# Kernel tuning notes

Measured on AMD Instinct MI355X. Metric: run time of the kernel, lower is better.

## Reference

```python
import jax, jax.numpy as jnp
import numpy as np

NUM_HEADS = 16
EMB = 1024
HEAD = 64
SEQ = 2048
BATCH = 4


def setup_inputs() -> dict:
    key = jax.random.key(0)
    ks = jax.random.split(key, 6)
    s = EMB ** -0.5
    x = jax.random.normal(ks[0], (BATCH, SEQ, EMB), dtype=jnp.float32)
    # per-head projection weights stacked: [H, E, D] (Linear(emb, head, bias=False) per head)
    Wq = jax.random.normal(ks[1], (NUM_HEADS, EMB, HEAD), dtype=jnp.float32) * s
    Wk = jax.random.normal(ks[2], (NUM_HEADS, EMB, HEAD), dtype=jnp.float32) * s
    Wv = jax.random.normal(ks[3], (NUM_HEADS, EMB, HEAD), dtype=jnp.float32) * s
    # output projection Linear(head*num_heads, emb): weight [E, H*D], bias [E]
    Wo = jax.random.normal(ks[4], (EMB, NUM_HEADS * HEAD), dtype=jnp.float32) * ((NUM_HEADS * HEAD) ** -0.5)
    bo = jax.random.normal(ks[5], (EMB,), dtype=jnp.float32) * 0.01
    return {"x": x, "Wq": Wq, "Wk": Wk, "Wv": Wv, "Wo": Wo, "bo": bo}


def reference(x, Wq, Wk, Wv, Wo, bo):
    B, S, E = x.shape
    scale = HEAD ** -0.5
    # batched per-head projections: [B, H, S, D]
    q = jnp.einsum('bse,hed->bhsd', x, Wq)
    k = jnp.einsum('bse,hed->bhsd', x, Wk)
    v = jnp.einsum('bse,hed->bhsd', x, Wv)
    scores = jnp.einsum('bhqd,bhkd->bhqk', q, k) * scale
    causal = jnp.tril(jnp.ones((S, S), dtype=bool))
    scores = jnp.where(causal, scores, jnp.finfo(scores.dtype).min)
    attn = jax.nn.softmax(scores, axis=-1)  # dropout disabled (eval/deterministic)
    ctx = jnp.einsum('bhqk,bhkd->bhqd', attn, v)
    # concat heads along last dim (head-major order, matching torch.cat)
    concat = ctx.transpose(0, 2, 1, 3).reshape(B, S, NUM_HEADS * HEAD)
    out = concat @ Wo.T + bo
    return out
```

## Files before the change

### kernel.cpp

```cpp
#include <hip/hip_runtime.h>

#define NHEADS 16
#define EMB 1024
#define HDIM 64
#define SEQ 2048
#define BATCH 4

typedef unsigned short u16;
typedef __attribute__((ext_vector_type(8))) __bf16 bf16x8;
typedef __attribute__((ext_vector_type(4))) float f32x4;

#if __has_builtin(__builtin_amdgcn_exp2f)
#define EXP2(x) __builtin_amdgcn_exp2f(x)
#else
#define EXP2(x) __expf((x)*0.69314718056f)
#endif
#define CL2E 0.18033688011112042f

__device__ __forceinline__ u16 f2bf(float f) {
  union { float f; unsigned u; } v; v.f = f;
  unsigned r = v.u + 0x7fffu + ((v.u >> 16) & 1u);
  return (u16)(r >> 16);
}
__device__ __forceinline__ unsigned pk2bf(float a, float b) {
  union { __bf16 h[2]; unsigned u; } x;
  x.h[0] = (__bf16)a; x.h[1] = (__bf16)b; return x.u;
}
__device__ __forceinline__ void gl16(const void* g, void* l) {
  __builtin_amdgcn_global_load_lds(
      (const __attribute__((address_space(1))) unsigned*)g,
      (__attribute__((address_space(3))) unsigned*)l, 16, 0, 0);
}

__global__ __launch_bounds__(256) void k_cvt(const float* __restrict__ in,
                                             u16* __restrict__ out, int n4) {
  int i = blockIdx.x * 256 + threadIdx.x;
  if (i >= n4) return;
  f32x4 v = *(const f32x4*)(in + (size_t)i * 4);
  uint2 o;
  o.x = (unsigned)f2bf(v[0]) | ((unsigned)f2bf(v[1]) << 16);
  o.y = (unsigned)f2bf(v[2]) | ((unsigned)f2bf(v[3]) << 16);
  *(uint2*)(out + (size_t)i * 4) = o;
}

__global__ __launch_bounds__(256) void k_packw(const float* __restrict__ Wq,
                                               const float* __restrict__ Wk,
                                               const float* __restrict__ Wv,
                                               u16* __restrict__ Wt) {
  const int mh = blockIdx.x;
  const int e0 = blockIdx.y * 64;
  const int mtx = mh >> 4, h = mh & 15;
  const float* W = (mtx == 0 ? Wq : (mtx == 1 ? Wk : Wv)) + (size_t)h * EMB * HDIM;
  __shared__ u16 sT[64][65];
  const int t = threadIdx.x;
  {
    int e = t >> 2, d0 = (t & 3) * 16;
#pragma unroll
    for (int jj = 0; jj < 4; jj++) {
      f32x4 v = *(const f32x4*)(W + (size_t)(e0 + e) * HDIM + d0 + jj * 4);
#pragma unroll
      for (int kk = 0; kk < 4; kk++) sT[e][d0 + jj * 4 + kk] = f2bf(v[kk]);
    }
  }
  __syncthreads();
  {
    int d = t >> 2, eb = (t & 3) * 16;
#pragma unroll
    for (int j = 0; j < 16; j++)
      Wt[(size_t)(mh * 64 + d) * EMB + e0 + eb + j] = sT[eb + j][d];
  }
}

__global__ __launch_bounds__(256) void k_gemm_qkv(const u16* __restrict__ Xb,
                                                  const u16* __restrict__ Wt,
                                                  u16* __restrict__ Q,
                                                  u16* __restrict__ K,
                                                  u16* __restrict__ V) {
  const int m0 = blockIdx.x * 128;
  const int n0 = blockIdx.y * 128;
  const int t = threadIdx.x;
  const int wave = t >> 6, lane = t & 63, lr = lane & 15, lg = lane >> 4;
  const int wr = (wave >> 1) * 64, wc = (wave & 1) * 64;

  __shared__ __align__(16) char sA[128 * 128];
  __shared__ __align__(16) char sB[128 * 128];

  const f32x4 fz = {0.f, 0.f, 0.f, 0.f};
  f32x4 acc[4][4];
#pragma unroll
  for (int i = 0; i < 4; i++)
#pragma unroll
    for (int j = 0; j < 4; j++) acc[i][j] = fz;

  for (int k0 = 0; k0 < EMB; k0 += 64) {
#pragma unroll
    for (int i = 0; i < 4; i++) {
      int rb = wave * 32 + i * 8;
      int row = rb + (lane >> 3);
      int gc = (lane & 7) ^ (row & 7);
      gl16(Xb + (size_t)(m0 + row) * EMB + k0 + gc * 8, sA + rb * 128);
      gl16(Wt + (size_t)(n0 + row) * EMB + k0 + gc * 8, sB + rb * 128);
    }
    __syncthreads();
    bf16x8 af[4][2], bfr[4][2];
#pragma unroll
    for (int mf = 0; mf < 4; mf++)
#pragma unroll
      for (int kf = 0; kf < 2; kf++) {
        int row = wr + mf * 16 + lr;
        af[mf][kf] = *(const bf16x8*)(sA + row * 128 + ((kf * 64 + lg * 16) ^ ((row & 7) << 4)));
      }
#pragma unroll
    for (int nf = 0; nf < 4; nf++)
#pragma unroll
      for (int kf = 0; kf < 2; kf++) {
        int row = wc + nf * 16 + lr;
        bfr[nf][kf] = *(const bf16x8*)(sB + row * 128 + ((kf * 64 + lg * 16) ^ ((row & 7) << 4)));
      }
#pragma unroll
    for (int kf = 0; kf < 2; kf++)
#pragma unroll
      for (int mf = 0; mf < 4; mf++)
#pragma unroll
        for (int nf = 0; nf < 4; nf++)
          acc[mf][nf] = __builtin_amdgcn_mfma_f32_16x16x32_bf16(af[mf][kf], bfr[nf][kf], acc[mf][nf], 0, 0, 0);
    __syncthreads();
  }

  const int b = m0 >> 11;
  const int s0 = m0 & 2047;
#pragma unroll
  for (int mf = 0; mf < 4; mf++)
#pragma unroll
    for (int nf = 0; nf < 4; nf++)
#pragma unroll
      for (int r = 0; r < 4; r++) {
        int row = wr + mf * 16 + lg * 4 + r;
        int n = n0 + wc + nf * 16 + lr;
        int mtx = n >> 10, h = (n >> 6) & 15, d = n & 63;
        u16* dst = (mtx == 0 ? Q : (mtx == 1 ? K : V));
        dst[((size_t)(b * NHEADS + h) * SEQ + s0 + row) * HDIM + d] = f2bf(acc[mf][nf][r]);
      }
}

__global__ __launch_bounds__(256, 3) void k_attn(const u16* __restrict__ Q,
                                                 const u16* __restrict__ K,
                                                 const u16* __restrict__ V,
                                                 u16* __restrict__ Cc) {
  const int bh = blockIdx.x;
  const int qt = 15 - (int)blockIdx.y;
  const int b = bh >> 4, h = bh & 15;
  const int t = threadIdx.x;
  const int wq = t >> 6, lane = t & 63, lr = lane & 15, lg = lane >> 4;
  const size_t base = (size_t)bh * SEQ * HDIM;

  __shared__ __align__(16) char sK[64 * 128];
  __shared__ __align__(16) char sV[64 * 128];
  __shared__ __align__(16) char sP[128 * 128];

#pragma unroll
  for (int i = 0; i < 4; i++) {
    int rb = wq * 32 + i * 8;
    int row = rb + (lane >> 3);
    int gc = (lane & 7) ^ (row & 7);
    gl16(Q + base + (size_t)(qt * 128 + row) * HDIM + gc * 8, sP + rb * 128);
  }
  __syncthreads();
  bf16x8 qf[2][2];
#pragma unroll
  for (int q2 = 0; q2 < 2; q2++)
#pragma unroll
    for (int kf = 0; kf < 2; kf++) {
      int row = wq * 32 + q2 * 16 + lr;
      qf[q2][kf] = *(const bf16x8*)(sP + row * 128 + ((kf * 64 + lg * 16) ^ ((row & 7) << 4)));
    }

  const f32x4 fz = {0.f, 0.f, 0.f, 0.f};
  f32x4 ot[4][2];
#pragma unroll
  for (int df = 0; df < 4; df++)
#pragma unroll
    for (int q2 = 0; q2 < 2; q2++) ot[df][q2] = fz;
  float m_[2] = {-1e30f, -1e30f}, l_[2] = {0.f, 0.f};

  const int nsteps = 2 * qt + 2;
  for (int step = 0; step < nsteps; step++) {
    const int k0 = step * 64;
    __syncthreads();
#pragma unroll
    for (int i = 0; i < 2; i++) {
      int rb = wq * 16 + i * 8;
      int row = rb + (lane >> 3);
      int gc = (lane & 7) ^ (row & 7);
      gl16(K + base + (size_t)(k0 + row) * HDIM + gc * 8, sK + rb * 128);
    }
    {
      const int kv = lane, d0 = wq * 16;
      const u16* vp = V + base + (size_t)(k0 + kv) * HDIM + d0;
      bf16x8 v0 = *(const bf16x8*)vp;
      bf16x8 v1 = *(const bf16x8*)(vp + 8);
#pragma unroll
      for (int j = 0; j < 8; j++) {
        int d = d0 + j, d2 = d0 + 8 + j;
        *(__bf16*)(sV + d * 128 + ((kv * 2) ^ ((d & 7) << 4))) = v0[j];
        *(__bf16*)(sV + d2 * 128 + ((kv * 2) ^ ((d2 & 7) << 4))) = v1[j];
      }
    }
    __syncthreads();

    f32x4 st[4][2];
#pragma unroll
    for (int kvf = 0; kvf < 4; kvf++)
#pragma unroll
      for (int q2 = 0; q2 < 2; q2++) st[kvf][q2] = fz;
#pragma unroll
    for (int kf = 0; kf < 2; kf++) {
      bf16x8 kfr[4];
#pragma unroll
      for (int kvf = 0; kvf < 4; kvf++) {
        int row = kvf * 16 + lr;
        kfr[kvf] = *(const bf16x8*)(sK + row * 128 + ((kf * 64 + lg * 16) ^ ((row & 7) << 4)));
      }
#pragma unroll
      for (int kvf = 0; kvf < 4; kvf++)
#pragma unroll
        for (int q2 = 0; q2 < 2; q2++)
          st[kvf][q2] = __builtin_amdgcn_mfma_f32_16x16x32_bf16(kfr[kvf], qf[q2][kf], st[kvf][q2], 0, 0, 0);
    }

    const bool diag = (k0 >= qt * 128);
#pragma unroll
    for (int q2 = 0; q2 < 2; q2++) {
      if (diag) {
        const int qg = qt * 128 + wq * 32 + q2 * 16 + lr;
#pragma unroll
        for (int kvf = 0; kvf < 4; kvf++)
#pragma unroll
          for (int r = 0; r < 4; r++)
            if (k0 + kvf * 16 + 4 * lg + r > qg) st[kvf][q2][r] = -3e38f;
      }
      float mx = -3e38f;
#pragma unroll
      for (int kvf = 0; kvf < 4; kvf++)
        mx = fmaxf(mx, fmaxf(fmaxf(st[kvf][q2][0], st[kvf][q2][1]),
                             fmaxf(st[kvf][q2][2], st[kvf][q2][3])));
      mx = fmaxf(mx, __shfl_xor(mx, 16));
      mx = fmaxf(mx, __shfl_xor(mx, 32));
      float mnew = fmaxf(m_[q2], mx);
      float alpha = EXP2((m_[q2] - mnew) * CL2E);
      m_[q2] = mnew;
      float nmc = -mnew * CL2E;
      float rs = 0.f;
      const int prow = wq * 32 + q2 * 16 + lr;
#pragma unroll
      for (int kvf = 0; kvf < 4; kvf++) {
        float p0 = EXP2(fmaf(st[kvf][q2][0], CL2E, nmc));
        float p1 = EXP2(fmaf(st[kvf][q2][1], CL2E, nmc));
        float p2 = EXP2(fmaf(st[kvf][q2][2], CL2E, nmc));
        float p3 = EXP2(fmaf(st[kvf][q2][3], CL2E, nmc));
        rs += (p0 + p1) + (p2 + p3);
        uint2 w;
        w.x = pk2bf(p0, p1);
        w.y = pk2bf(p2, p3);
        *(uint2*)(sP + prow * 128 + ((kvf * 32 + lg * 8) ^ ((prow & 7) << 4))) = w;
      }
      rs += __shfl_xor(rs, 16);
      rs += __shfl_xor(rs, 32);
      l_[q2] = l_[q2] * alpha + rs;
#pragma unroll
      for (int df = 0; df < 4; df++) ot[df][q2] *= alpha;
    }

#pragma unroll
    for (int kf = 0; kf < 2; kf++) {
      bf16x8 pf[2], vf[4];
#pragma unroll
      for (int q2 = 0; q2 < 2; q2++) {
        int row = wq * 32 + q2 * 16 + lr;
        pf[q2] = *(const bf16x8*)(sP + row * 128 + ((kf * 64 + lg * 16) ^ ((row & 7) << 4)));
      }
#pragma unroll
      for (int df = 0; df < 4; df++) {
        int row = df * 16 + lr;
        vf[df] = *(const bf16x8*)(sV + row * 128 + ((kf * 64 + lg * 16) ^ ((row & 7) << 4)));
      }
#pragma unroll
      for (int df = 0; df < 4; df++)
#pragma unroll
        for (int q2 = 0; q2 < 2; q2++)
          ot[df][q2] = __builtin_amdgcn_mfma_f32_16x16x32_bf16(vf[df], pf[q2], ot[df][q2], 0, 0, 0);
    }
  }

#pragma unroll
  for (int q2 = 0; q2 < 2; q2++) {
    float inv = 1.0f / l_[q2];
    int s = qt * 128 + wq * 32 + q2 * 16 + lr;
#pragma unroll
    for (int df = 0; df < 4; df++) {
      uint2 w;
      w.x = pk2bf(ot[df][q2][0] * inv, ot[df][q2][1] * inv);
      w.y = pk2bf(ot[df][q2][2] * inv, ot[df][q2][3] * inv);
      *(uint2*)(Cc + ((size_t)b * SEQ + s) * (NHEADS * HDIM) + h * HDIM + df * 16 + 4 * lg) = w;
    }
  }
}

__global__ __launch_bounds__(256) void k_gemm_out(const u16* __restrict__ Cc,
                                                  const u16* __restrict__ Wob,
                                                  const float* __restrict__ bo,
                                                  float* __restrict__ out) {
  const int m0 = blockIdx.x * 128;
  const int n0 = blockIdx.y * 128;
  const int t = threadIdx.x;
  const int wave = t >> 6, lane = t & 63, lr = lane & 15, lg = lane >> 4;
  const int wr = (wave >> 1) * 64, wc = (wave & 1) * 64;

  __shared__ __align__(16) char sA[128 * 128];
  __shared__ __align__(16) char sB[128 * 128];

  const f32x4 fz = {0.f, 0.f, 0.f, 0.f};
  f32x4 acc[4][4];
#pragma unroll
  for (int i = 0; i < 4; i++)
#pragma unroll
    for (int j = 0; j < 4; j++) acc[i][j] = fz;

  for (int k0 = 0; k0 < EMB; k0 += 64) {
#pragma unroll
    for (int i = 0; i < 4; i++) {
      int rb = wave * 32 + i * 8;
      int row = rb + (lane >> 3);
      int gc = (lane & 7) ^ (row & 7);
      gl16(Cc + (size_t)(m0 + row) * EMB + k0 + gc * 8, sA + rb * 128);
      gl16(Wob + (size_t)(n0 + row) * EMB + k0 + gc * 8, sB + rb * 128);
    }
    __syncthreads();
    bf16x8 af[4][2], bfr[4][2];
#pragma unroll
    for (int mf = 0; mf < 4; mf++)
#pragma unroll
      for (int kf = 0; kf < 2; kf++) {
        int row = wr + mf * 16 + lr;
        af[mf][kf] = *(const bf16x8*)(sA + row * 128 + ((kf * 64 + lg * 16) ^ ((row & 7) << 4)));
      }
#pragma unroll
    for (int nf = 0; nf < 4; nf++)
#pragma unroll
      for (int kf = 0; kf < 2; kf++) {
        int row = wc + nf * 16 + lr;
        bfr[nf][kf] = *(const bf16x8*)(sB + row * 128 + ((kf * 64 + lg * 16) ^ ((row & 7) << 4)));
      }
#pragma unroll
    for (int kf = 0; kf < 2; kf++)
#pragma unroll
      for (int mf = 0; mf < 4; mf++)
#pragma unroll
        for (int nf = 0; nf < 4; nf++)
          acc[mf][nf] = __builtin_amdgcn_mfma_f32_16x16x32_bf16(af[mf][kf], bfr[nf][kf], acc[mf][nf], 0, 0, 0);
    __syncthreads();
  }

  float bv[4];
#pragma unroll
  for (int nf = 0; nf < 4; nf++) bv[nf] = bo[n0 + wc + nf * 16 + lr];
#pragma unroll
  for (int mf = 0; mf < 4; mf++)
#pragma unroll
    for (int nf = 0; nf < 4; nf++)
#pragma unroll
      for (int r = 0; r < 4; r++) {
        int row = wr + mf * 16 + lg * 4 + r;
        int n = n0 + wc + nf * 16 + lr;
        out[(size_t)(m0 + row) * EMB + n] = acc[mf][nf][r] + bv[nf];
      }
}

extern "C" void kernel_launch(void* const* d_in, const int* in_sizes, int n_in,
                              void* d_out, int out_size, void* d_ws, size_t ws_size,
                              hipStream_t stream) {
  const float* x  = (const float*)d_in[0];
  const float* Wq = (const float*)d_in[1];
  const float* Wk = (const float*)d_in[2];
  const float* Wv = (const float*)d_in[3];
  const float* Wo = (const float*)d_in[4];
  const float* bo = (const float*)d_in[5];
  float* out = (float*)d_out;

  char* ws = (char*)d_ws;
  const size_t SZ_XB  = (size_t)8192 * 1024 * 2;
  const size_t SZ_WT  = (size_t)3072 * 1024 * 2;
  const size_t SZ_WOB = (size_t)1024 * 1024 * 2;
  const size_t SZ_QKV = (size_t)64 * 2048 * 64 * 2;
  u16* Xb  = (u16*)(ws);
  u16* Wt  = (u16*)(ws + SZ_XB);
  u16* Wob = (u16*)(ws + SZ_XB + SZ_WT);
  u16* Qb  = (u16*)(ws + SZ_XB + SZ_WT + SZ_WOB);
  u16* Kb  = (u16*)(ws + SZ_XB + SZ_WT + SZ_WOB + SZ_QKV);
  u16* Vb  = (u16*)(ws + SZ_XB + SZ_WT + SZ_WOB + 2 * SZ_QKV);
  u16* Cc  = (u16*)(ws + SZ_XB + SZ_WT + SZ_WOB + 3 * SZ_QKV);

  k_cvt<<<8192, 256, 0, stream>>>(x, Xb, 2097152);
  k_cvt<<<1024, 256, 0, stream>>>(Wo, Wob, 262144);
  k_packw<<<dim3(48, 16), 256, 0, stream>>>(Wq, Wk, Wv, Wt);
  k_gemm_qkv<<<dim3(64, 24), 256, 0, stream>>>(Xb, Wt, Qb, Kb, Vb);
  k_attn<<<dim3(64, 16), 256, 0, stream>>>(Qb, Kb, Vb, Cc);
  k_gemm_out<<<dim3(64, 8), 256, 0, stream>>>(Cc, Wob, bo, out);
}
```

Before: 174.1 us.

## Rewrite QKV GEMM as 8-wave 256x192 double-buffered pipelined kernel

Replaces the 128x128-tile QKV projection GEMM with a 512-thread kernel that computes 256x192 tiles. It double-buffers LDS (112 KB dynamic) so global-to-LDS loads for the next K step overlap MFMA work on the current one, using explicit vmcnt waits, barriers and setprio. Block indices are remapped for L2 locality. The goal is to hide load latency and raise data reuse per tile, at the cost of large LDS use, lower occupancy and fragile hand-written wait counts.

Measured after the change: 172.2 us. Within noise of the previous version (-1.1%).

```diff
diff --git a/kernel.cpp b/kernel.cpp
--- a/kernel.cpp
+++ b/kernel.cpp
@@ -16,6 +16,12 @@
 #define EXP2(x) __expf((x)*0.69314718056f)
 #endif
 #define CL2E 0.18033688011112042f
+
+#define BARRIER() __builtin_amdgcn_s_barrier()
+#define SB0() __builtin_amdgcn_sched_barrier(0)
+#define PRIO1() __builtin_amdgcn_s_setprio(1)
+#define PRIO0() __builtin_amdgcn_s_setprio(0)
+#define VMCNT(n) asm volatile("s_waitcnt vmcnt(" #n ")" ::: "memory")
 
 __device__ __forceinline__ u16 f2bf(float f) {
   union { float f; unsigned u; } v; v.f = f;
@@ -71,75 +77,127 @@
   }
 }
 
-__global__ __launch_bounds__(256) void k_gemm_qkv(const u16* __restrict__ Xb,
-                                                  const u16* __restrict__ Wt,
-                                                  u16* __restrict__ Q,
-                                                  u16* __restrict__ K,
-                                                  u16* __restrict__ V) {
-  const int m0 = blockIdx.x * 128;
-  const int n0 = blockIdx.y * 128;
+__global__ __launch_bounds__(512, 2) void k_gemm_qkv8(const u16* __restrict__ Xb,
+                                                      const u16* __restrict__ Wt,
+                                                      u16* __restrict__ Q,
+                                                      u16* __restrict__ K,
+                                                      u16* __restrict__ V) {
+  extern __shared__ __align__(16) char smem[];
+  const int bid = blockIdx.x;
+  const int l = (bid & 7) * 64 + (bid >> 3);
+  const int mt = l & 31, nt = l >> 5;
+  const int m0 = mt * 256, n0 = nt * 192;
+
   const int t = threadIdx.x;
   const int wave = t >> 6, lane = t & 63, lr = lane & 15, lg = lane >> 4;
-  const int wr = (wave >> 1) * 64, wc = (wave & 1) * 64;
-
-  __shared__ __align__(16) char sA[128 * 128];
-  __shared__ __align__(16) char sB[128 * 128];
+  const int wr = (wave >> 2) * 128;
+  const int wc = (wave & 3) * 48;
 
   const f32x4 fz = {0.f, 0.f, 0.f, 0.f};
-  f32x4 acc[4][4];
-#pragma unroll
-  for (int i = 0; i < 4; i++)
-#pragma unroll
-    for (int j = 0; j < 4; j++) acc[i][j] = fz;
-
-  for (int k0 = 0; k0 < EMB; k0 += 64) {
-#pragma unroll
-    for (int i = 0; i < 4; i++) {
-      int rb = wave * 32 + i * 8;
-      int row = rb + (lane >> 3);
-      int gc = (lane & 7) ^ (row & 7);
-      gl16(Xb + (size_t)(m0 + row) * EMB + k0 + gc * 8, sA + rb * 128);
-      gl16(Wt + (size_t)(n0 + row) * EMB + k0 + gc * 8, sB + rb * 128);
-    }
-    __syncthreads();
-    bf16x8 af[4][2], bfr[4][2];
+  f32x4 acc[8][3];
+#pragma unroll
+  for (int i = 0; i < 8; i++)
+#pragma unroll
+    for (int j = 0; j < 3; j++) acc[i][j] = fz;
+
+  bf16x8 af[4][2], bfr[3][2];
+
+  auto SROUND = [&](char* ldsbase, int rbase, const u16* src, int gRowBase, int kt) {
+    int rs = rbase + wave * 8;
+    int row = rs + (lane >> 3);
+    int gc = (lane & 7) ^ (row & 7);
+    gl16(src + (size_t)(gRowBase + row) * EMB + kt * 64 + gc * 8, ldsbase + rs * 128);
+  };
+  auto LOADA = [&](const char* bA, int mh) {
 #pragma unroll
     for (int mf = 0; mf < 4; mf++)
 #pragma unroll
       for (int kf = 0; kf < 2; kf++) {
-        int row = wr + mf * 16 + lr;
-        af[mf][kf] = *(const bf16x8*)(sA + row * 128 + ((kf * 64 + lg * 16) ^ ((row & 7) << 4)));
-      }
-#pragma unroll
-    for (int nf = 0; nf < 4; nf++)
+        int row = wr + mh * 64 + mf * 16 + lr;
+        af[mf][kf] = *(const bf16x8*)(bA + row * 128 + ((kf * 64 + lg * 16) ^ ((row & 7) << 4)));
+      }
+  };
+  auto LOADB = [&](const char* bB) {
+#pragma unroll
+    for (int nf = 0; nf < 3; nf++)
 #pragma unroll
       for (int kf = 0; kf < 2; kf++) {
         int row = wc + nf * 16 + lr;
-        bfr[nf][kf] = *(const bf16x8*)(sB + row * 128 + ((kf * 64 + lg * 16) ^ ((row & 7) << 4)));
-      }
-#pragma unroll
-    for (int kf = 0; kf < 2; kf++)
-#pragma unroll
-      for (int mf = 0; mf < 4; mf++)
-#pragma unroll
-        for (int nf = 0; nf < 4; nf++)
-          acc[mf][nf] = __builtin_amdgcn_mfma_f32_16x16x32_bf16(af[mf][kf], bfr[nf][kf], acc[mf][nf], 0, 0, 0);
-    __syncthreads();
-  }
+        bfr[nf][kf] = *(const bf16x8*)(bB + row * 128 + ((kf * 64 + lg * 16) ^ ((row & 7) << 4)));
+      }
+  };
+
+#define MFMAPH(MH)                                                                         \
+  do {                                                                                     \
+    _Pragma("unroll") for (int kf = 0; kf < 2; kf++)                                       \
+    _Pragma("unroll") for (int mf = 0; mf < 4; mf++)                                       \
+    _Pragma("unroll") for (int nf = 0; nf < 3; nf++)                                       \
+      acc[(MH)*4 + mf][nf] = __builtin_amdgcn_mfma_f32_16x16x32_bf16(                      \
+          af[mf][kf], bfr[nf][kf], acc[(MH)*4 + mf][nf], 0, 0, 0);                         \
+  } while (0)
+
+  const int NT = EMB / 64;
+  {
+    char* nA = smem;
+    char* nB = smem + 32768;
+    SROUND(nB, 0, Wt, n0, 0); SROUND(nB, 64, Wt, n0, 0); SROUND(nB, 128, Wt, n0, 0);
+    SROUND(nA, 0, Xb, m0, 0);
+    SROUND(nA, 64, Xb, m0, 0); SROUND(nA, 128, Xb, m0, 0); SROUND(nA, 192, Xb, m0, 0);
+  }
+  VMCNT(0);
+  BARRIER();
+
+  for (int tt = 0; tt < NT - 1; tt++) {
+    const int cb = tt & 1, nb = cb ^ 1;
+    char* bA = smem + cb * 57344;
+    char* bB = bA + 32768;
+    char* nA = smem + nb * 57344;
+    char* nB = nA + 32768;
+    SROUND(nB, 0, Wt, n0, tt + 1);
+    SROUND(nB, 64, Wt, n0, tt + 1);
+    SROUND(nB, 128, Wt, n0, tt + 1);
+    SROUND(nA, 0, Xb, m0, tt + 1);
+    LOADA(bA, 0);
+    LOADB(bB);
+    VMCNT(4);
+    BARRIER(); SB0();
+    PRIO1(); MFMAPH(0); PRIO0();
+    BARRIER();
+    SROUND(nA, 64, Xb, m0, tt + 1);
+    SROUND(nA, 128, Xb, m0, tt + 1);
+    SROUND(nA, 192, Xb, m0, tt + 1);
+    LOADA(bA, 1);
+    VMCNT(2);
+    BARRIER(); SB0();
+    PRIO1(); MFMAPH(1); PRIO0();
+    BARRIER();
+  }
+  {
+    char* bA = smem + ((NT - 1) & 1) * 57344;
+    char* bB = bA + 32768;
+    LOADA(bA, 0);
+    LOADB(bB);
+    VMCNT(0);
+    BARRIER(); SB0();
+    PRIO1(); MFMAPH(0); PRIO0();
+    LOADA(bA, 1);
+    PRIO1(); MFMAPH(1); PRIO0();
+  }
+#undef MFMAPH
 
   const int b = m0 >> 11;
   const int s0 = m0 & 2047;
 #pragma unroll
-  for (int mf = 0; mf < 4; mf++)
-#pragma unroll
-    for (int nf = 0; nf < 4; nf++)
+  for (int am = 0; am < 8; am++)
+#pragma unroll
+    for (int nf = 0; nf < 3; nf++)
 #pragma unroll
       for (int r = 0; r < 4; r++) {
-        int row = wr + mf * 16 + lg * 4 + r;
+        int row = wr + am * 16 + lg * 4 + r;
         int n = n0 + wc + nf * 16 + lr;
         int mtx = n >> 10, h = (n >> 6) & 15, d = n & 63;
         u16* dst = (mtx == 0 ? Q : (mtx == 1 ? K : V));
-        dst[((size_t)(b * NHEADS + h) * SEQ + s0 + row) * HDIM + d] = f2bf(acc[mf][nf][r]);
+        dst[((size_t)(b * NHEADS + h) * SEQ + s0 + row) * HDIM + d] = f2bf(acc[am][nf][r]);
       }
 }
 
@@ -403,7 +461,7 @@
   k_cvt<<<8192, 256, 0, stream>>>(x, Xb, 2097152);
   k_cvt<<<1024, 256, 0, stream>>>(Wo, Wob, 262144);
   k_packw<<<dim3(48, 16), 256, 0, stream>>>(Wq, Wk, Wv, Wt);
-  k_gemm_qkv<<<dim3(64, 24), 256, 0, stream>>>(Xb, Wt, Qb, Kb, Vb);
+  k_gemm_qkv8<<<512, 512, 114688, stream>>>(Xb, Wt, Qb, Kb, Vb);
   k_attn<<<dim3(64, 16), 256, 0, stream>>>(Qb, Kb, Vb, Cc);
   k_gemm_out<<<dim3(64, 8), 256, 0, stream>>>(Cc, Wob, bo, out);
 }
```
